# Optimization experiments

Measured on AMD Instinct MI355X. Metric: run time of the kernel, lower is better.

## Reference

```python
import jax, jax.numpy as jnp
import numpy as np

EPS = 1e-5
NUM_HEADS = 16


def rms_norm(x, w):
    v = jnp.mean(x * x, axis=-1, keepdims=True)
    return x * jax.lax.rsqrt(v + EPS) * w


def rotate_half_interleaved(x):
    # pairs (x0,x1) -> (-x1, x0), interleaved layout
    x1 = x[..., 0::2]
    x2 = x[..., 1::2]
    return jnp.stack([-x2, x1], axis=-1).reshape(x.shape)


def setup_inputs() -> dict:
    key = jax.random.key(0)
    ks = jax.random.split(key, 6)
    B, N, C = 2, 2048, 2048
    D = C // NUM_HEADS
    s = 1.0 / np.sqrt(C)
    return {
        "x": jax.random.normal(ks[0], (B, N, C), jnp.float32),
        "w_qkv": jax.random.normal(ks[1], (3 * C, C), jnp.float32) * s,
        "q_norm_w": jnp.ones((C,), jnp.float32),
        "k_norm_w": jnp.ones((C,), jnp.float32),
        "cos": jnp.cos(jax.random.normal(ks[2], (N, D), jnp.float32)),
        "sin": jnp.sin(jax.random.normal(ks[3], (N, D), jnp.float32)),
        "w_proj": jax.random.normal(ks[4], (C, C), jnp.float32) * s,
        "b_proj": jnp.zeros((C,), jnp.float32),
    }


def reference(x, w_qkv, q_norm_w, k_norm_w, cos, sin, w_proj, b_proj):
    B, N, C = x.shape
    H = NUM_HEADS
    D = C // H
    scale = D ** -0.5

    qkv = jnp.einsum("bnc,fc->bnf", x, w_qkv).reshape(B, N, 3, C)
    q, k, v = qkv[:, :, 0], qkv[:, :, 1], qkv[:, :, 2]

    # RMSNorm over full channel dim C (as in the torch module), then head split
    q = rms_norm(q, q_norm_w).reshape(B, N, H, D)
    k = rms_norm(k, k_norm_w).reshape(B, N, H, D)
    v = v.reshape(B, N, H, D)

    # rotary embedding (head_first=False layout [B,N,H,D])
    c = cos[None, :, None, :]
    s = sin[None, :, None, :]
    q = q * c + rotate_half_interleaved(q) * s
    k = k * c + rotate_half_interleaved(k) * s

    attn = jnp.einsum("bnhd,bmhd->bhnm", q, k) * scale  # [B,H,N,N]
    attn = jax.nn.softmax(attn, axis=-1)
    out = jnp.einsum("bhnm,bmhd->bnhd", attn, v).reshape(B, N, C)
    return jnp.einsum("bnc,oc->bno", out, w_proj) + b_proj
```

## Files before the change

kernel.cpp:

```cpp
#include <hip/hip_runtime.h>
#include <stdint.h>

typedef unsigned short u16;
typedef unsigned int   u32;
typedef _Float16 f16_t;
typedef f16_t f16x8 __attribute__((ext_vector_type(8)));
typedef float  f32x4  __attribute__((ext_vector_type(4)));

#define BB 2
#define NN 2048
#define CC 2048
#define HH 16
#define DD 128
#define FF 6144
#define MM 4096

__device__ __forceinline__ u16 f2h(float f){
    f16_t h = (f16_t)f;
    return __builtin_bit_cast(u16, h);
}
__device__ __forceinline__ float h2f(u16 b){
    return (float)__builtin_bit_cast(f16_t, b);
}
__device__ __forceinline__ f32x4 MFMA(f16x8 a, f16x8 b, f32x4 c){
    return __builtin_amdgcn_mfma_f32_16x16x32_f16(a, b, c, 0, 0, 0);
}
__device__ __forceinline__ void gld16(const void* g, void* l){
    __builtin_amdgcn_global_load_lds(
        (const __attribute__((address_space(1))) void*)(g),
        (__attribute__((address_space(3))) void*)(l), 16, 0, 0);
}

__global__ void k_f2h(const float* __restrict__ a, u16* __restrict__ o, int n4){
    int i = blockIdx.x * blockDim.x + threadIdx.x;
    int stride = gridDim.x * blockDim.x;
    for (; i < n4; i += stride){
        float4 v = ((const float4*)a)[i];
        ushort4 r; r.x = f2h(v.x); r.y = f2h(v.y); r.z = f2h(v.z); r.w = f2h(v.w);
        ((ushort4*)o)[i] = r;
    }
}

template<int OUTH>
__global__ __launch_bounds__(256) void k_gemm_bt(
    const u16* __restrict__ A, const u16* __restrict__ Bw,
    float* __restrict__ outf, u16* __restrict__ outb,
    const float* __restrict__ bias, int M, int N, int K)
{
    __shared__ u16 As[3][128 * 32];
    __shared__ u16 Bs[3][128 * 32];
    const int tid  = threadIdx.x;
    const int brow = blockIdx.y * 128;
    const int bcol = blockIdx.x * 128;
    const int w = tid >> 6, lane = tid & 63;
    const int wr = w >> 1, wc = w & 1;
    const int l15 = lane & 15, g = lane >> 4;
    const int sr  = tid >> 2;
    const int scz = ((tid & 3) ^ ((tid >> 3) & 3)) * 8;
    const int gx  = (g ^ ((l15 >> 1) & 3)) * 8;

    f32x4 acc[4][4];
    #pragma unroll
    for (int i = 0; i < 4; i++)
        #pragma unroll
        for (int j = 0; j < 4; j++){
            f32x4 z = {0.f, 0.f, 0.f, 0.f};
            acc[i][j] = z;
        }

    auto stage = [&](int buf, int k0){
        gld16(&Bw[(size_t)(bcol + sr) * K + k0 + scz],      &Bs[buf][w * 512]);
        gld16(&Bw[(size_t)(bcol + sr + 64) * K + k0 + scz], &Bs[buf][2048 + w * 512]);
        gld16(&A [(size_t)(brow + sr) * K + k0 + scz],      &As[buf][w * 512]);
        gld16(&A [(size_t)(brow + sr + 64) * K + k0 + scz], &As[buf][2048 + w * 512]);
    };

    stage(0, 0);
    stage(1, 32);
    int c = 0;
    for (int k0 = 0; k0 < K; k0 += 32){
        __builtin_amdgcn_sched_barrier(0);
        __builtin_amdgcn_s_barrier();
        __builtin_amdgcn_sched_barrier(0);
        int ct = c + 2; if (ct >= 3) ct -= 3;
        if (k0 + 64 < K){
            stage(ct, k0 + 64);
            asm volatile("s_waitcnt vmcnt(8)" ::: "memory");
        } else if (k0 + 32 < K){
            asm volatile("s_waitcnt vmcnt(4)" ::: "memory");
        } else {
            asm volatile("s_waitcnt vmcnt(0)" ::: "memory");
        }
        __builtin_amdgcn_sched_barrier(0);
        __builtin_amdgcn_s_barrier();
        __builtin_amdgcn_sched_barrier(0);
        f16x8 fb[4];
        #pragma unroll
        for (int j = 0; j < 4; j++){
            int row = wc * 64 + j * 16 + l15;
            fb[j] = *(const f16x8*)&Bs[c][row * 32 + gx];
        }
        #pragma unroll
        for (int i = 0; i < 4; i++){
            int row = wr * 64 + i * 16 + l15;
            f16x8 fa = *(const f16x8*)&As[c][row * 32 + gx];
            #pragma unroll
            for (int j = 0; j < 4; j++) acc[i][j] = MFMA(fa, fb[j], acc[i][j]);
        }
        c = (c + 1 == 3) ? 0 : c + 1;
    }

    #pragma unroll
    for (int i = 0; i < 4; i++){
        #pragma unroll
        for (int j = 0; j < 4; j++){
            int colg = bcol + wc * 64 + j * 16 + l15;
            #pragma unroll
            for (int r = 0; r < 4; r++){
                int rowg = brow + wr * 64 + i * 16 + 4 * g + r;
                float v = acc[i][j][r];
                if (OUTH) outb[(size_t)rowg * N + colg] = f2h(v);
                else      outf[(size_t)rowg * N + colg] = v + bias[colg];
            }
        }
    }
}

__global__ __launch_bounds__(256) void k_norm_rope(
    const u16* __restrict__ qkv, const float* __restrict__ qw, const float* __restrict__ kw,
    const float* __restrict__ cosb, const float* __restrict__ sinb,
    u16* __restrict__ qout, u16* __restrict__ kout)
{
    const int m = blockIdx.x;
    const int b = m >> 11;
    const int n = m & 2047;
    const int t = threadIdx.x;
    const size_t base = (size_t)m * FF;
    const int e0 = t * 8;
    const float SCL = 0.08838834764831845f * 1.4426950408889634f;

    float qv[8], kvv[8];
    uint4 qa = *(const uint4*)&qkv[base + e0];
    uint4 ka = *(const uint4*)&qkv[base + CC + e0];
    {
        u32 aa[4] = {qa.x, qa.y, qa.z, qa.w};
        u32 bb[4] = {ka.x, ka.y, ka.z, ka.w};
        #pragma unroll
        for (int i = 0; i < 4; i++){
            qv[2*i]   = h2f((u16)(aa[i] & 0xffff));
            qv[2*i+1] = h2f((u16)(aa[i] >> 16));
            kvv[2*i]   = h2f((u16)(bb[i] & 0xffff));
            kvv[2*i+1] = h2f((u16)(bb[i] >> 16));
        }
    }
    float sq = 0.f, sk = 0.f;
    #pragma unroll
    for (int i = 0; i < 8; i++){ sq += qv[i]*qv[i]; sk += kvv[i]*kvv[i]; }
    #pragma unroll
    for (int o = 32; o > 0; o >>= 1){ sq += __shfl_xor(sq, o); sk += __shfl_xor(sk, o); }
    __shared__ float red[8];
    if ((t & 63) == 0){ red[(t >> 6)*2] = sq; red[(t >> 6)*2 + 1] = sk; }
    __syncthreads();
    sq = red[0] + red[2] + red[4] + red[6];
    sk = red[1] + red[3] + red[5] + red[7];
    const float rq = rsqrtf(sq * (1.f / 2048.f) + 1e-5f);
    const float rk = rsqrtf(sk * (1.f / 2048.f) + 1e-5f);

    const int h  = t >> 4;
    const int d0 = (t & 15) * 8;
    const float* cp = cosb + (size_t)n * DD + d0;
    const float* sp = sinb + (size_t)n * DD + d0;
    float qo[8], ko[8];
    #pragma unroll
    for (int j = 0; j < 8; j += 2){
        float c0 = cp[j], c1 = cp[j+1], s0 = sp[j], s1 = sp[j+1];
        float x0 = qv[j]   * rq * qw[e0 + j];
        float x1 = qv[j+1] * rq * qw[e0 + j + 1];
        qo[j]   = (x0 * c0 - x1 * s0) * SCL;
        qo[j+1] = (x1 * c1 + x0 * s1) * SCL;
        float y0 = kvv[j]   * rk * kw[e0 + j];
        float y1 = kvv[j+1] * rk * kw[e0 + j + 1];
        ko[j]   = y0 * c0 - y1 * s0;
        ko[j+1] = y1 * c1 + y0 * s1;
    }
    const size_t obase = ((size_t)(b * HH + h) * NN + n) * DD + d0;
    uint4 pq, pk;
    pq.x = (u32)f2h(qo[0]) | ((u32)f2h(qo[1]) << 16);
    pq.y = (u32)f2h(qo[2]) | ((u32)f2h(qo[3]) << 16);
    pq.z = (u32)f2h(qo[4]) | ((u32)f2h(qo[5]) << 16);
    pq.w = (u32)f2h(qo[6]) | ((u32)f2h(qo[7]) << 16);
    pk.x = (u32)f2h(ko[0]) | ((u32)f2h(ko[1]) << 16);
    pk.y = (u32)f2h(ko[2]) | ((u32)f2h(ko[3]) << 16);
    pk.z = (u32)f2h(ko[4]) | ((u32)f2h(ko[5]) << 16);
    pk.w = (u32)f2h(ko[6]) | ((u32)f2h(ko[7]) << 16);
    *(uint4*)&qout[obase] = pq;
    *(uint4*)&kout[obase] = pk;
}

__global__ __launch_bounds__(256) void k_vtrans(const u16* __restrict__ qkv, u16* __restrict__ Vt){
    __shared__ u16 t[64 * 66];
    const int bh = blockIdx.z;
    const int b = bh >> 4, h = bh & 15;
    const int n0 = blockIdx.x * 64, d0 = blockIdx.y * 64;
    const int tid = threadIdx.x;
    const int q = tid & 7, p = tid >> 3;
    #pragma unroll
    for (int it = 0; it < 2; it++){
        int r = p + it * 32;
        const u16* src = qkv + (size_t)(b * NN + n0 + r) * FF + 2 * CC + h * DD + d0 + q * 8;
        uint4 v = *(const uint4*)src;
        u32* dst = (u32*)&t[r * 66 + q * 8];
        dst[0] = v.x; dst[1] = v.y; dst[2] = v.z; dst[3] = v.w;
    }
    __syncthreads();
    #pragma unroll
    for (int it = 0; it < 2; it++){
        int rd = p + it * 32;
        u16 o[8];
        #pragma unroll
        for (int j = 0; j < 8; j++) o[j] = t[(q * 8 + j) * 66 + rd];
        *(uint4*)(Vt + ((size_t)bh * DD + d0 + rd) * NN + n0 + q * 8) = *(uint4*)o;
    }
}

__global__ __launch_bounds__(256, 2) void k_attn5(
    const u16* __restrict__ Q, const u16* __restrict__ Kt, const u16* __restrict__ Vt2,
    u16* __restrict__ O)
{
    __shared__ u16 Kbuf[2][8192];
    __shared__ u16 Vbuf[2][8192];
    const int tid = threadIdx.x;
    const int w = tid >> 6, lane = tid & 63;
    const int l15 = lane & 15, g = lane >> 4;
    const int flat = blockIdx.x;
    const int lid  = (flat & 7) * 64 + (flat >> 3);
    const int qb = lid & 15;
    const int h  = (lid >> 4) & 15;
    const int b  = lid >> 8;
    const size_t hb  = (size_t)(b * HH + h) * NN * DD;
    const size_t hbT = (size_t)(b * HH + h) * DD * NN;
    const int qbase = qb * 128 + w * 32;
    const int mperm = 8 * (l15 >> 2) + (l15 & 3);

    f16x8 qf[2][4];
    #pragma unroll
    for (int u = 0; u < 2; u++){
        const u16* qrow = Q + hb + (size_t)(qbase + u * 16 + l15) * DD;
        #pragma unroll
        for (int c = 0; c < 4; c++)
            qf[u][c] = *(const f16x8*)(qrow + c * 32 + 8 * g);
    }

    f32x4 oacc[2][8];
    #pragma unroll
    for (int u = 0; u < 2; u++)
        #pragma unroll
        for (int tb = 0; tb < 8; tb++){ f32x4 z = {0.f,0.f,0.f,0.f}; oacc[u][tb] = z; }
    float lsum0 = 0.f, lsum1 = 0.f;

    auto stage = [&](int buf, int kv0){
        #pragma unroll
        for (int it = 0; it < 8; it++){
            int s = it * 4 + w;
            if (s < 16){
                int hh = s >> 3, t = (s >> 2) & 1, c = s & 3;
                gld16(&Kt[hb + (size_t)(kv0 + 32 * hh + 4 * t + mperm) * DD + 32 * c + 8 * g],
                      &Kbuf[buf][s * 512]);
            } else {
                int s2 = s - 16;
                int hh = s2 >> 3, tb = s2 & 7;
                gld16(&Vt2[hbT + (size_t)(tb * 16 + l15) * NN + kv0 + 32 * hh + 8 * g],
                      &Vbuf[buf][s2 * 512]);
            }
        }
    };

    int cur = 0;
    stage(0, 0);
    for (int kv0 = 0; kv0 < NN; kv0 += 64){
        __syncthreads();
        if (kv0 + 64 < NN) stage(cur ^ 1, kv0 + 64);
        const u16* kb = &Kbuf[cur][0] + lane * 8;
        const u16* vb = &Vbuf[cur][0] + lane * 8;
        #pragma unroll
        for (int hh = 0; hh < 2; hh++){
            f32x4 st00 = {0,0,0,0}, st01 = {0,0,0,0}, st10 = {0,0,0,0}, st11 = {0,0,0,0};
            __builtin_amdgcn_s_setprio(1);
            #pragma unroll
            for (int c = 0; c < 4; c++){
                f16x8 kf0 = *(const f16x8*)(kb + (hh * 8 + c) * 512);
                f16x8 kf1 = *(const f16x8*)(kb + (hh * 8 + 4 + c) * 512);
                st00 = MFMA(kf0, qf[0][c], st00);
                st01 = MFMA(kf0, qf[1][c], st01);
                st10 = MFMA(kf1, qf[0][c], st10);
                st11 = MFMA(kf1, qf[1][c], st11);
            }
            __builtin_amdgcn_s_setprio(0);
            f16x8 pf0, pf1;
            #pragma unroll
            for (int r = 0; r < 4; r++){
                float e00 = exp2f(st00[r]), e10 = exp2f(st10[r]);
                float e01 = exp2f(st01[r]), e11 = exp2f(st11[r]);
                lsum0 += e00 + e10;
                lsum1 += e01 + e11;
                pf0[r] = (f16_t)e00; pf0[r + 4] = (f16_t)e10;
                pf1[r] = (f16_t)e01; pf1[r + 4] = (f16_t)e11;
            }
            __builtin_amdgcn_s_setprio(1);
            #pragma unroll
            for (int tb = 0; tb < 8; tb++){
                f16x8 vf = *(const f16x8*)(vb + (hh * 8 + tb) * 512);
                oacc[0][tb] = MFMA(pf0, vf, oacc[0][tb]);
                oacc[1][tb] = MFMA(pf1, vf, oacc[1][tb]);
            }
            __builtin_amdgcn_s_setprio(0);
        }
        cur ^= 1;
    }

    lsum0 += __shfl_xor(lsum0, 16); lsum0 += __shfl_xor(lsum0, 32);
    lsum1 += __shfl_xor(lsum1, 16); lsum1 += __shfl_xor(lsum1, 32);
    float linv0 = 1.f / lsum0, linv1 = 1.f / lsum1;
    float li0[4], li1[4];
    #pragma unroll
    for (int r = 0; r < 4; r++){
        li0[r] = __shfl(linv0, 4 * g + r);
        li1[r] = __shfl(linv1, 4 * g + r);
    }

    #pragma unroll
    for (int tb = 0; tb < 8; tb++){
        #pragma unroll
        for (int r = 0; r < 4; r++){
            int q0 = qbase + 4 * g + r;
            O[(size_t)(b * NN + q0) * CC + h * DD + tb * 16 + l15] = f2h(oacc[0][tb][r] * li0[r]);
            int q1 = qbase + 16 + 4 * g + r;
            O[(size_t)(b * NN + q1) * CC + h * DD + tb * 16 + l15] = f2h(oacc[1][tb][r] * li1[r]);
        }
    }
}

extern "C" void kernel_launch(void* const* d_in, const int* in_sizes, int n_in,
                              void* d_out, int out_size, void* d_ws, size_t ws_size,
                              hipStream_t stream) {
    const float* x      = (const float*)d_in[0];
    const float* w_qkv  = (const float*)d_in[1];
    const float* qw     = (const float*)d_in[2];
    const float* kw     = (const float*)d_in[3];
    const float* cosb   = (const float*)d_in[4];
    const float* sinb   = (const float*)d_in[5];
    const float* w_proj = (const float*)d_in[6];
    const float* b_proj = (const float*)d_in[7];
    float* out = (float*)d_out;

    const size_t sz_xh   = (size_t)MM * CC * 2;
    const size_t sz_wqkv = (size_t)FF * CC * 2;
    const size_t sz_wprj = (size_t)CC * CC * 2;
    const size_t sz_qkv  = (size_t)MM * FF * 2;
    const size_t sz_t    = (size_t)BB * HH * NN * DD * 2;
    const size_t need = sz_xh + sz_wqkv + sz_wprj + sz_qkv + sz_t*3 + sz_xh;
    if (ws_size < need) return;

    char* ws = (char*)d_ws;
    size_t off = 0;
    auto alloc = [&](size_t bytes){ void* p = ws + off; off += (bytes + 255) & ~(size_t)255; return p; };
    u16* x_h     = (u16*)alloc(sz_xh);
    u16* wqkv_h  = (u16*)alloc(sz_wqkv);
    u16* wprj_h  = (u16*)alloc(sz_wprj);
    u16* qkv     = (u16*)alloc(sz_qkv);
    u16* qr      = (u16*)alloc(sz_t);
    u16* kr      = (u16*)alloc(sz_t);
    u16* vt2     = (u16*)alloc(sz_t);
    u16* ob      = (u16*)alloc(sz_xh);

    k_f2h<<<2048, 256, 0, stream>>>(x, x_h, MM * CC / 4);
    k_f2h<<<2048, 256, 0, stream>>>(w_qkv, wqkv_h, FF * CC / 4);
    k_f2h<<<1024, 256, 0, stream>>>(w_proj, wprj_h, CC * CC / 4);
    k_gemm_bt<1><<<dim3(FF / 128, MM / 128), 256, 0, stream>>>(
        x_h, wqkv_h, nullptr, qkv, nullptr, MM, FF, CC);
    k_norm_rope<<<MM, 256, 0, stream>>>(qkv, qw, kw, cosb, sinb, qr, kr);
    k_vtrans<<<dim3(NN / 64, DD / 64, BB * HH), 256, 0, stream>>>(qkv, vt2);
    k_attn5<<<512, 256, 0, stream>>>(qr, kr, vt2, ob);
    k_gemm_bt<0><<<dim3(CC / 128, MM / 128), 256, 0, stream>>>(
        ob, wprj_h, out, nullptr, b_proj, MM, CC, CC);
}
```

Before: 318.6 us.

## Load GEMM A-operand directly into registers, keep only B in LDS

The GEMM no longer stages the A tile through shared memory. Each wave loads its A fragments straight from global memory into registers, double-buffered across two k-steps, and only B stays in the triple-buffered LDS ring. The goal is to halve LDS traffic and footprint so occupancy can rise, with launch bounds now hinting 3 blocks per CU. In exchange, A rows are read redundantly by the two column-waves with narrower, less-coalesced accesses, register pressure goes up, and the vmcnt wait counts have to stay exactly right.

```diff
diff --git a/kernel.cpp b/kernel.cpp
--- a/kernel.cpp
+++ b/kernel.cpp
@@ -30,6 +30,7 @@
         (const __attribute__((address_space(1))) void*)(g),
         (__attribute__((address_space(3))) void*)(l), 16, 0, 0);
 }
+#define SB0() __builtin_amdgcn_sched_barrier(0)
 
 __global__ void k_f2h(const float* __restrict__ a, u16* __restrict__ o, int n4){
     int i = blockIdx.x * blockDim.x + threadIdx.x;
@@ -42,12 +43,11 @@
 }
 
 template<int OUTH>
-__global__ __launch_bounds__(256) void k_gemm_bt(
+__global__ __launch_bounds__(256, 3) void k_gemm_bt(
     const u16* __restrict__ A, const u16* __restrict__ Bw,
     float* __restrict__ outf, u16* __restrict__ outb,
     const float* __restrict__ bias, int M, int N, int K)
 {
-    __shared__ u16 As[3][128 * 32];
     __shared__ u16 Bs[3][128 * 32];
     const int tid  = threadIdx.x;
     const int brow = blockIdx.y * 128;
@@ -68,45 +68,60 @@
             acc[i][j] = z;
         }
 
-    auto stage = [&](int buf, int k0){
+    const u16* arow[4];
+    #pragma unroll
+    for (int i = 0; i < 4; i++)
+        arow[i] = &A[(size_t)(brow + wr * 64 + i * 16 + l15) * K + 8 * g];
+
+    auto stageB = [&](int buf, int k0){
         gld16(&Bw[(size_t)(bcol + sr) * K + k0 + scz],      &Bs[buf][w * 512]);
         gld16(&Bw[(size_t)(bcol + sr + 64) * K + k0 + scz], &Bs[buf][2048 + w * 512]);
-        gld16(&A [(size_t)(brow + sr) * K + k0 + scz],      &As[buf][w * 512]);
-        gld16(&A [(size_t)(brow + sr + 64) * K + k0 + scz], &As[buf][2048 + w * 512]);
     };
-
-    stage(0, 0);
-    stage(1, 32);
-    int c = 0;
-    for (int k0 = 0; k0 < K; k0 += 32){
-        __builtin_amdgcn_sched_barrier(0);
-        __builtin_amdgcn_s_barrier();
-        __builtin_amdgcn_sched_barrier(0);
-        int ct = c + 2; if (ct >= 3) ct -= 3;
-        if (k0 + 64 < K){
-            stage(ct, k0 + 64);
-            asm volatile("s_waitcnt vmcnt(8)" ::: "memory");
-        } else if (k0 + 32 < K){
-            asm volatile("s_waitcnt vmcnt(4)" ::: "memory");
-        } else {
-            asm volatile("s_waitcnt vmcnt(0)" ::: "memory");
-        }
-        __builtin_amdgcn_sched_barrier(0);
-        __builtin_amdgcn_s_barrier();
-        __builtin_amdgcn_sched_barrier(0);
+    auto loadA = [&](int k0, f16x8 (&af)[4]){
+        #pragma unroll
+        for (int i = 0; i < 4; i++)
+            af[i] = *(const f16x8*)(arow[i] + k0);
+    };
+    auto compute = [&](int buf, const f16x8 (&af)[4]){
         f16x8 fb[4];
         #pragma unroll
         for (int j = 0; j < 4; j++){
             int row = wc * 64 + j * 16 + l15;
-            fb[j] = *(const f16x8*)&Bs[c][row * 32 + gx];
-        }
-        #pragma unroll
-        for (int i = 0; i < 4; i++){
-            int row = wr * 64 + i * 16 + l15;
-            f16x8 fa = *(const f16x8*)&As[c][row * 32 + gx];
+            fb[j] = *(const f16x8*)&Bs[buf][row * 32 + gx];
+        }
+        #pragma unroll
+        for (int i = 0; i < 4; i++)
             #pragma unroll
-            for (int j = 0; j < 4; j++) acc[i][j] = MFMA(fa, fb[j], acc[i][j]);
-        }
+            for (int j = 0; j < 4; j++) acc[i][j] = MFMA(af[i], fb[j], acc[i][j]);
+    };
+
+    f16x8 afa[4], afb[4];
+    stageB(0, 0);
+    stageB(1, 32);
+    loadA(0, afa);
+    int c = 0;
+    const int nK = K >> 5;
+    for (int t = 0; t < nK; t += 2){
+        SB0(); __builtin_amdgcn_s_barrier(); SB0();
+        int ct = c + 2; if (ct >= 3) ct -= 3;
+        if (t + 2 < nK) stageB(ct, (t + 2) * 32);
+        loadA((t + 1) * 32, afb);
+        SB0();
+        if (t + 2 < nK) asm volatile("s_waitcnt vmcnt(6)" ::: "memory");
+        else            asm volatile("s_waitcnt vmcnt(4)" ::: "memory");
+        SB0(); __builtin_amdgcn_s_barrier(); SB0();
+        compute(c, afa);
+        c = (c + 1 == 3) ? 0 : c + 1;
+        SB0(); __builtin_amdgcn_s_barrier(); SB0();
+        ct = c + 2; if (ct >= 3) ct -= 3;
+        if (t + 3 < nK) stageB(ct, (t + 3) * 32);
+        if (t + 2 < nK) loadA((t + 2) * 32, afa);
+        SB0();
+        if (t + 3 < nK)      asm volatile("s_waitcnt vmcnt(6)" ::: "memory");
+        else if (t + 2 < nK) asm volatile("s_waitcnt vmcnt(4)" ::: "memory");
+        else                 asm volatile("s_waitcnt vmcnt(0)" ::: "memory");
+        SB0(); __builtin_amdgcn_s_barrier(); SB0();
+        compute(c, afb);
         c = (c + 1 == 3) ? 0 : c + 1;
     }
 
```

After: 432.9 us. 35.9% more time.
